# Optimization experiments

Hardware: AMD Instinct MI355X
Metric: run time of the kernel (lower is better)

Reference implementation:

```python
import jax, jax.numpy as jnp
import numpy as np

C, T, V, H, DQ = 64, 128, 25, 3, 32  # channels, frames, joints, heads, qkv_dim
EPS = 1e-5
LRELU_SLOPE = 0.1


def pos_embed(channels, num_frames, num_joints):
    # DSTA-Net style sinusoidal Pos_Embed: position index is the joint id, tiled over frames
    pos = np.tile(np.arange(num_joints, dtype=np.float32), num_frames)[:, None]  # (T*V, 1)
    div = np.exp(np.arange(0, channels, 2, dtype=np.float32) * -(np.log(10000.0) / channels))
    pe = np.zeros((num_frames * num_joints, channels), dtype=np.float32)
    pe[:, 0::2] = np.sin(pos * div)
    pe[:, 1::2] = np.cos(pos * div)
    pe = pe.reshape(num_frames, num_joints, channels).transpose(2, 0, 1)[None]  # (1, C, T, V)
    return jnp.asarray(pe)


def batchnorm2d(x, gamma, beta):
    # training-mode BN over (N, T, V) per channel, biased variance (torch default)
    m = x.mean(axis=(0, 2, 3), keepdims=True)
    v = x.var(axis=(0, 2, 3), keepdims=True)
    return (x - m) * jax.lax.rsqrt(v + EPS) * gamma[None, :, None, None] + beta[None, :, None, None]


def setup_inputs() -> dict:
    key = jax.random.key(0)
    ks = jax.random.split(key, 4)
    N = 64
    return {
        "x": jax.random.normal(ks[0], (N, C, T, V), jnp.float32),
        "Wqkv": jax.random.normal(ks[1], (2 * H * DQ, C), jnp.float32) * 0.05,   # 1x1 conv weight
        "bqkv": jnp.zeros((2 * H * DQ,), jnp.float32),
        "alphas": jnp.ones((1, H, 1, 1), jnp.float32),
        "att0s": jax.random.uniform(ks[2], (1, H, V, V), jnp.float32) / V,
        "Wout": jax.random.normal(ks[3], (C, H * C, 1, 5), jnp.float32) * 0.02,  # (1,5) temporal conv
        "bout": jnp.zeros((C,), jnp.float32),
        "gamma": jnp.ones((C,), jnp.float32),
        "beta": jnp.zeros((C,), jnp.float32),
    }


def reference(x, Wqkv, bqkv, alphas, att0s, Wout, bout, gamma, beta):
    N = x.shape[0]
    xs = x + pos_embed(C, T, V)                                   # pes(x) + x
    qk = jnp.einsum('nctv,oc->notv', xs, Wqkv) + bqkv[None, :, None, None]
    qk = qk.reshape(N, 2 * H, DQ, T, V)
    q, k = qk[:, :H], qk[:, H:]
    # tanh-gated joint-attention, no softmax
    att = jnp.tanh(jnp.einsum('nhctu,nhctv->nhuv', q, k) / (DQ * T)) * alphas + att0s
    y = jnp.einsum('nctu,nhuv->nhctv', x, att).reshape(N, H * C, T, V)
    y = jax.lax.conv_general_dilated(
        y, Wout, window_strides=(1, 1), padding=((0, 0), (2, 2)),
        dimension_numbers=('NCHW', 'OIHW', 'NCHW')) + bout[None, :, None, None]
    y = batchnorm2d(y, gamma, beta)
    return jax.nn.leaky_relu(y + x, LRELU_SLOPE)                  # ress is identity (in==out)
```

## Files before the change

kernel.cpp:

```cpp
#include <hip/hip_runtime.h>
#include <hip/hip_bf16.h>


#define WS_ATT    0
#define WS_STATS  120000
#define WS_WBF    120128
#define WS_WP     150848
#define WS_BP     156992
#define WS_PE     157184
#define WS_SPART  158784
#define WS_ATTBF  166976

typedef __attribute__((ext_vector_type(8))) short short8;
typedef __attribute__((ext_vector_type(4))) float floatx4;

__device__ __forceinline__ float us2f(unsigned short u) {
    union { unsigned int i; float f; } w; w.i = ((unsigned int)u) << 16; return w.f;
}
__device__ __forceinline__ unsigned short f2us(float f) {
    __hip_bfloat16_raw r = __float2bfloat16(f); return r.x;
}

__device__ __forceinline__ int swz(int col, int byteoff) {
    return col * 128 + ((((byteoff >> 4) ^ (col & 7)) << 4) | (byteoff & 15));
}

__device__ __forceinline__ void bar_lgkm() {
    asm volatile("s_waitcnt lgkmcnt(0)" ::: "memory");
    __builtin_amdgcn_s_barrier();
}

__global__ void k_wprep(const float* __restrict__ Wout, const float* __restrict__ Wqkv,
                        const float* __restrict__ bqkv, unsigned short* __restrict__ Abf,
                        unsigned short* __restrict__ Wp, float* __restrict__ bp,
                        float* __restrict__ pe)
{
    int i = blockIdx.x * 256 + threadIdx.x;
    if (i < 61440) {
        int tap = i / 12288, rem = i % 12288;
        int o = rem / 192, hc = rem % 192;
        Abf[i] = f2us(Wout[o * 960 + hc * 5 + tap]);
    } else if (i < 73728) {
        int j = i - 61440;
        int np = j >> 6, c = j & 63;
        int h = np >> 6, qk = (np >> 5) & 1, cp = np & 31;
        Wp[j] = f2us(Wqkv[(qk * 96 + h * 32 + cp) * 64 + c]);
    } else if (i < 73920) {
        int np = i - 73728;
        int h = np >> 6, qk = (np >> 5) & 1, cp = np & 31;
        bp[np] = bqkv[qk * 96 + h * 32 + cp];
    } else if (i < 75520) {
        int e = i - 73920;
        int c = e / 25, v = e % 25;
        int ii = c >> 1;
        float d = expf(-(float)(2 * ii) * (9.210340371976184f / 64.0f));
        float a = (float)v * d;
        pe[e] = (c & 1) ? cosf(a) : sinf(a);
    }
}

#define CPAD 112

__global__ __launch_bounds__(256, 2) void k_att(
    const float* __restrict__ x, const unsigned short* __restrict__ Wp,
    const float* __restrict__ bp, const float* __restrict__ peg,
    float* __restrict__ att_raw)
{
    __shared__ unsigned short xs_s[2][CPAD * 64];
    __shared__ unsigned short qk_s[3 * CPAD * 64];
    __shared__ float pe_s[1600];

    const int tid  = threadIdx.x;
    const int lane = tid & 63, wv = tid >> 6;
    const int l16  = lane & 15, quad = lane >> 4;
    const int n    = blockIdx.y;
    const int tb0  = blockIdx.x * 16;

    const int col_a = lane;
    const int col_b = 64 + lane;
    const int va = (col_a < 25) ? col_a : (col_a < 50 ? col_a - 25 : col_a - 50);
    const int vb = (col_b < 75) ? col_b - 50 : col_b - 75;
    char* qkb = (char*)qk_s;

    float ra0[8], ra1[8], rb0[8], rb1[8];

#define LOADCH(CH) do {                                                         \
    const int g0_ = (tb0 + (CH) * 4) * 25;                                      \
    _Pragma("unroll")                                                           \
    for (int cp8 = 0; cp8 < 8; ++cp8) {                                         \
        const float* xp0_ = x + (size_t)(n * 64 + (wv * 8 + cp8) * 2) * 3200 + g0_; \
        const float* xp1_ = xp0_ + 3200;                                        \
        ra0[cp8] = xp0_[col_a]; ra1[cp8] = xp1_[col_a];                         \
        if (lane < 36) { rb0[cp8] = xp0_[col_b]; rb1[cp8] = xp1_[col_b]; }      \
    } } while (0)

    LOADCH(0);

    for (int e = tid; e < 1600; e += 256) pe_s[e] = peg[e];

    short8 afrag[3][2];
    float  biasr[3][4];
    #pragma unroll
    for (int mt = 0; mt < 3; ++mt) {
        int row = (3 * wv + mt) * 16 + l16;
        #pragma unroll
        for (int kk = 0; kk < 2; ++kk)
            afrag[mt][kk] = *(const short8*)(Wp + row * 64 + kk * 32 + quad * 8);
        #pragma unroll
        for (int reg = 0; reg < 4; ++reg)
            biasr[mt][reg] = bp[(3 * wv + mt) * 16 + quad * 4 + reg];
    }

    floatx4 qacc[3][2][2];
    #pragma unroll
    for (int h = 0; h < 3; ++h)
        #pragma unroll
        for (int a = 0; a < 2; ++a)
            #pragma unroll
            for (int b = 0; b < 2; ++b)
                qacc[h][a][b] = (floatx4){0.0f, 0.0f, 0.0f, 0.0f};

    bar_lgkm();

    #pragma unroll
    for (int ch = 0; ch < 4; ++ch) {
        char* xsb = (char*)xs_s[ch & 1];

        #pragma unroll
        for (int cp8 = 0; cp8 < 8; ++cp8) {
            const int cpair = wv * 8 + cp8, c0 = cpair * 2;
            unsigned int pk =
                (unsigned int)f2us(ra0[cp8] + pe_s[c0 * 25 + va]) |
                ((unsigned int)f2us(ra1[cp8] + pe_s[c0 * 25 + 25 + va]) << 16);
            *(unsigned int*)(xsb + swz(col_a, cpair * 4)) = pk;
            if (lane < 36) {
                pk = (unsigned int)f2us(rb0[cp8] + pe_s[c0 * 25 + vb]) |
                     ((unsigned int)f2us(rb1[cp8] + pe_s[c0 * 25 + 25 + vb]) << 16);
                *(unsigned int*)(xsb + swz(col_b, cpair * 4)) = pk;
            }
        }
        if (ch < 3) LOADCH(ch + 1);
        bar_lgkm();

        #pragma unroll
        for (int nt = 0; nt < 7; ++nt) {
            const int col = nt * 16 + l16;
            short8 b0 = *(const short8*)(xsb + swz(col, quad * 16));
            short8 b1 = *(const short8*)(xsb + swz(col, 64 + quad * 16));
            #pragma unroll
            for (int mt = 0; mt < 3; ++mt) {
                floatx4 acc = (floatx4){0.0f, 0.0f, 0.0f, 0.0f};
                acc = __builtin_amdgcn_mfma_f32_16x16x32_bf16(afrag[mt][0], b0, acc, 0, 0, 0);
                acc = __builtin_amdgcn_mfma_f32_16x16x32_bf16(afrag[mt][1], b1, acc, 0, 0, 0);
                const int np  = (3 * wv + mt) * 16 + quad * 4;
                const int h   = np >> 6;
                const int off = (np & 63) * 2;
                unsigned long long pk =
                      (unsigned long long)f2us(acc[0] + biasr[mt][0])
                    | ((unsigned long long)f2us(acc[1] + biasr[mt][1]) << 16)
                    | ((unsigned long long)f2us(acc[2] + biasr[mt][2]) << 32)
                    | ((unsigned long long)f2us(acc[3] + biasr[mt][3]) << 48);
                *(unsigned long long*)(qkb + h * (CPAD * 128) + swz(col, off)) = pk;
            }
        }
        bar_lgkm();

        const int tcol = wv * 25;
        #pragma unroll
        for (int h = 0; h < 3; ++h) {
            char* qh = qkb + h * (CPAD * 128);
            short8 qa0 = *(const short8*)(qh + swz(tcol + l16,      quad * 16));
            short8 qa1 = *(const short8*)(qh + swz(tcol + 16 + l16, quad * 16));
            short8 kb0 = *(const short8*)(qh + swz(tcol + l16,      64 + quad * 16));
            short8 kb1 = *(const short8*)(qh + swz(tcol + 16 + l16, 64 + quad * 16));
            qacc[h][0][0] = __builtin_amdgcn_mfma_f32_16x16x32_bf16(qa0, kb0, qacc[h][0][0], 0, 0, 0);
            qacc[h][0][1] = __builtin_amdgcn_mfma_f32_16x16x32_bf16(qa0, kb1, qacc[h][0][1], 0, 0, 0);
            qacc[h][1][0] = __builtin_amdgcn_mfma_f32_16x16x32_bf16(qa1, kb0, qacc[h][1][0], 0, 0, 0);
            qacc[h][1][1] = __builtin_amdgcn_mfma_f32_16x16x32_bf16(qa1, kb1, qacc[h][1][1], 0, 0, 0);
        }
    }

    __syncthreads();
    float* att_s = (float*)qk_s;
    for (int e = tid; e < 1875; e += 256) att_s[e] = 0.0f;
    __syncthreads();
    #pragma unroll
    for (int h = 0; h < 3; ++h) {
        #pragma unroll
        for (int ut = 0; ut < 2; ++ut) {
            #pragma unroll
            for (int vt = 0; vt < 2; ++vt) {
                const int v = vt * 16 + l16;
                if (v < 25) {
                    const int ub = ut * 16 + quad * 4;
                    #pragma unroll
                    for (int reg = 0; reg < 4; ++reg) {
                        const int u = ub + reg;
                        if (u < 25)
                            atomicAdd(&att_s[h * 625 + u * 25 + v], qacc[h][ut][vt][reg]);
                    }
                }
            }
        }
    }
    __syncthreads();
    for (int e = tid; e < 1875; e += 256)
        atomicAdd(&att_raw[(size_t)n * 1875 + e], att_s[e]);
}

__global__ void k_attfin(const float* __restrict__ att_raw,
                         unsigned short* __restrict__ attbf,
                         const float* __restrict__ alphas,
                         const float* __restrict__ att0s)
{
    int idx = blockIdx.x * 256 + threadIdx.x;
    if (idx >= 64 * 3 * 25 * 40) return;
    int u = idx % 40;
    int r = idx / 40;
    int v = r % 25;
    int nh = r / 25;
    int h = nh % 3;
    unsigned short val = 0;
    if (u < 25) {
        float a = att_raw[nh * 625 + u * 25 + v];
        val = f2us(tanhf(a * (1.0f / 4096.0f)) * alphas[h] + att0s[h * 625 + u * 25 + v]);
    }
    attbf[idx] = val;
}

__global__ __launch_bounds__(256, 2) void k_conv(
    const float* __restrict__ x, const unsigned short* __restrict__ Abf,
    const float* __restrict__ bout, const unsigned short* __restrict__ attbf,
    float* __restrict__ out, float* __restrict__ spart)
{
    __shared__ unsigned short yT[11136];
    __shared__ unsigned short x_sb[4096];
    __shared__ unsigned short attT[3000];
    __shared__ float stats_s[128];

    const int tid = threadIdx.x;
    const int lane = tid & 63, wv = tid >> 6;
    const int quad = lane >> 4, l16 = lane & 15;
    const int n = blockIdx.y;
    const int t0 = blockIdx.x * 2;
    char* xsb = (char*)x_sb;

    const int o0 = wv * 16;
    short8 areg[5][6];
    const unsigned short* apb = Abf + (o0 + l16) * 192 + quad * 8;
    #pragma unroll
    for (int tap = 0; tap < 5; ++tap)
        #pragma unroll
        for (int kk = 0; kk < 6; ++kk)
            areg[tap][kk] = *(const short8*)(apb + tap * 12288 + kk * 32);
    float bo[4];
    #pragma unroll
    for (int reg = 0; reg < 4; ++reg) bo[reg] = bout[o0 + quad * 4 + reg];

    if (tid < 128) stats_s[tid] = 0.0f;

    for (int e = tid; e < 896; e += 256) {
        int c = e / 14, r = e % 14;
        int t = r / 7, u = 25 + r % 7;
        *(unsigned short*)(xsb + swz(c, (t * 32 + u) * 2)) = 0;
    }
    for (int e = tid; e < 1600; e += 256) {
        int c = e / 25, j = e % 25;
        const float2 xv = *(const float2*)(x + (size_t)(n * 64 + c) * 3200 + t0 * 25 + 2 * j);
        int i0 = 2 * j, i1 = i0 + 1;
        int p0 = (i0 / 25) * 32 + (i0 % 25);
        int p1 = (i1 / 25) * 32 + (i1 % 25);
        *(unsigned short*)(xsb + swz(c, p0 * 2)) = f2us(xv.x);
        *(unsigned short*)(xsb + swz(c, p1 * 2)) = f2us(xv.y);
    }
    {
        const uint4* src = (const uint4*)(attbf + (size_t)n * 3000);
        uint4* dst = (uint4*)attT;
        for (int e = tid; e < 375; e += 256) dst[e] = src[e];
    }
    for (int e = tid; e < 1536; e += 256) {
        int t = e / 768, r = e % 768;
        int vi = r / 192, hc = r % 192;
        int vv = (vi < 2) ? vi : (25 + vi);
        int phys = (t * 29 + vv) * 192 + (((hc >> 3) ^ (vv & 7)) << 3) + (hc & 7);
        yT[phys] = 0;
    }
    __syncthreads();

    {
        const int c0 = wv * 16;
        const int crow = c0 + l16;
        short8 af[2];
        #pragma unroll
        for (int t = 0; t < 2; ++t)
            af[t] = *(const short8*)(xsb + swz(crow, (t * 32 + quad * 8) * 2));
        short8 bfr[3][2];
        #pragma unroll
        for (int h = 0; h < 3; ++h)
            #pragma unroll
            for (int nt = 0; nt < 2; ++nt) {
                int v = nt * 16 + l16; if (v > 24) v = 24;
                bfr[h][nt] = *(const short8*)&attT[(h * 25 + v) * 40 + quad * 8];
            }
        #pragma unroll
        for (int t = 0; t < 2; ++t)
            #pragma unroll
            for (int h = 0; h < 3; ++h)
                #pragma unroll
                for (int nt = 0; nt < 2; ++nt) {
                    floatx4 d = (floatx4){0.0f, 0.0f, 0.0f, 0.0f};
                    d = __builtin_amdgcn_mfma_f32_16x16x32_bf16(af[t], bfr[h][nt], d, 0, 0, 0);
                    const int v = nt * 16 + l16;
                    if (v < 25) {
                        const int vv = v + 2;
                        const int hc = h * 64 + c0 + quad * 4;
                        const int phys = (t * 29 + vv) * 192 + (((hc >> 3) ^ (vv & 7)) << 3) + (hc & 7);
                        unsigned long long pk =
                              (unsigned long long)f2us(d[0])
                            | ((unsigned long long)f2us(d[1]) << 16)
                            | ((unsigned long long)f2us(d[2]) << 32)
                            | ((unsigned long long)f2us(d[3]) << 48);
                        *(unsigned long long*)&yT[phys] = pk;
                    }
                }
    }

    bar_lgkm();

    #pragma unroll
    for (int np = 0; np < 2; ++np) {
        const int colA = np * 32 + l16;
        const int colB = np * 32 + 16 + l16;
        const bool okA = colA < 50, okB = colB < 50;
        const int ccA = okA ? colA : 49, ccB = okB ? colB : 49;
        const int tcA = ccA / 25, vcA = ccA % 25;
        const int tcB = ccB / 25, vcB = ccB % 25;
        floatx4 accA = {0,0,0,0}, accB = {0,0,0,0};
        #pragma unroll
        for (int tap = 0; tap < 5; ++tap) {
            const int vvA = vcA + tap, vvB = vcB + tap;
            const int roA = (tcA * 29 + vvA) * 192, vxA = vvA & 7;
            const int roB = (tcB * 29 + vvB) * 192, vxB = vvB & 7;
            #pragma unroll
            for (int kk = 0; kk < 6; ++kk) {
                short8 bA = *(const short8*)&yT[roA + (((kk * 4 + quad) ^ vxA) << 3)];
                short8 bB = *(const short8*)&yT[roB + (((kk * 4 + quad) ^ vxB) << 3)];
                accA = __builtin_amdgcn_mfma_f32_16x16x32_bf16(areg[tap][kk], bA, accA, 0, 0, 0);
                accB = __builtin_amdgcn_mfma_f32_16x16x32_bf16(areg[tap][kk], bB, accB, 0, 0, 0);
            }
        }

#define EPIS(ACC, OK, TC, VC)                                                  \
        do {                                                                   \
            float vr[4];                                                       \
            _Pragma("unroll")                                                  \
            for (int reg = 0; reg < 4; ++reg)                                  \
                vr[reg] = (OK) ? ACC[reg] + bo[reg] : 0.0f;                    \
            if (OK) {                                                          \
                float* op = out + (size_t)(n * 64 + o0 + quad * 4) * 3200      \
                            + (t0 + (TC)) * 25 + (VC);                         \
                _Pragma("unroll")                                              \
                for (int reg = 0; reg < 4; ++reg)                              \
                    op[(size_t)reg * 3200] = vr[reg];                          \
            }                                                                  \
            _Pragma("unroll")                                                  \
            for (int reg = 0; reg < 4; ++reg) {                                \
                float s1 = vr[reg], s2 = vr[reg] * vr[reg];                    \
                _Pragma("unroll")                                              \
                for (int m = 1; m < 16; m <<= 1) {                             \
                    s1 += __shfl_xor(s1, m);                                   \
                    s2 += __shfl_xor(s2, m);                                   \
                }                                                              \
                if (l16 == 0) {                                                \
                    atomicAdd(&stats_s[o0 + quad * 4 + reg], s1);              \
                    atomicAdd(&stats_s[64 + o0 + quad * 4 + reg], s2);         \
                }                                                              \
            }                                                                  \
        } while (0)

        EPIS(accA, okA, tcA, vcA);
        EPIS(accB, okB, tcB, vcB);
#undef EPIS
    }

    __syncthreads();
    if (tid < 128)
        atomicAdd(&spart[(size_t)blockIdx.x * 128 + tid], stats_s[tid]);
}

__global__ void k_statsred(const float* __restrict__ spart, float* __restrict__ stats)
{
    int o = threadIdx.x;
    float s = 0.0f;
    #pragma unroll 8
    for (int t = 0; t < 64; ++t) s += spart[t * 128 + o];
    stats[o] = s;
}

__global__ void k_final(const float* __restrict__ stats, const float4* __restrict__ x4,
                        const float* __restrict__ gamma, const float* __restrict__ beta,
                        float4* __restrict__ out4)
{
    int idx = blockIdx.x * 256 + threadIdx.x;
    if (idx >= 3276800) return;
    int o = (idx / 800) & 63;
    const float inv = 1.0f / 204800.0f;
    float m   = stats[o] * inv;
    float ex2 = stats[64 + o] * inv;
    float var = ex2 - m * m;
    float r = rsqrtf(var + 1e-5f);
    float g = gamma[o], bb = beta[o];
    float4 v = out4[idx];
    float4 xx = x4[idx];
    float4 res;
    float t;
    t = (v.x - m) * r * g + bb + xx.x; res.x = fmaxf(t, 0.1f * t);
    t = (v.y - m) * r * g + bb + xx.y; res.y = fmaxf(t, 0.1f * t);
    t = (v.z - m) * r * g + bb + xx.z; res.z = fmaxf(t, 0.1f * t);
    t = (v.w - m) * r * g + bb + xx.w; res.w = fmaxf(t, 0.1f * t);
    out4[idx] = res;
}

extern "C" void kernel_launch(void* const* d_in, const int* in_sizes, int n_in,
                              void* d_out, int out_size, void* d_ws, size_t ws_size,
                              hipStream_t stream)
{
    const float* x      = (const float*)d_in[0];
    const float* Wqkv   = (const float*)d_in[1];
    const float* bqkv   = (const float*)d_in[2];
    const float* alphas = (const float*)d_in[3];
    const float* att0s  = (const float*)d_in[4];
    const float* Wout   = (const float*)d_in[5];
    const float* bout   = (const float*)d_in[6];
    const float* gamma  = (const float*)d_in[7];
    const float* beta   = (const float*)d_in[8];
    float* ws  = (float*)d_ws;
    float* out = (float*)d_out;
    unsigned short* Abf   = (unsigned short*)(ws + WS_WBF);
    unsigned short* Wp    = (unsigned short*)(ws + WS_WP);
    float*          bp    = ws + WS_BP;
    float*          pe    = ws + WS_PE;
    float*          spart = ws + WS_SPART;
    unsigned short* attbf = (unsigned short*)(ws + WS_ATTBF);

    hipMemsetAsync(d_ws, 0, (size_t)120000 * sizeof(float), stream);
    hipMemsetAsync(spart, 0, (size_t)8192 * sizeof(float), stream);

    k_wprep   <<<296, 256, 0, stream>>>(Wout, Wqkv, bqkv, Abf, Wp, bp, pe);
    k_att     <<<dim3(8, 64),  256, 0, stream>>>(x, Wp, bp, pe, ws + WS_ATT);
    k_attfin  <<<750, 256, 0, stream>>>(ws + WS_ATT, attbf, alphas, att0s);
    k_conv    <<<dim3(64, 64), 256, 0, stream>>>(x, Abf, bout, attbf, out, spart);
    k_statsred<<<1, 128, 0, stream>>>(spart, ws + WS_STATS);
    k_final   <<<12800, 256, 0, stream>>>(ws + WS_STATS, (const float4*)x,
                                          gamma, beta, (float4*)out);
}
```

Measured before the change: 307.8 us.

## Make conv blocks loop over 8 frame pairs with prefetched x and fused stats

k_conv now has each block handle 16 frames as 8 iterations over frame pairs, instead of launching one block per pair. Each block loads the conv weights into registers once and reuses them across iterations, and it prefetches the next pair's x into registers while the MFMA conv runs. BN statistics are kept in registers and reduced once at the end, then atomically added straight into the global stats, which removes the spart buffer, its memset and the k_statsred launch. The trade-off is fewer blocks (512 instead of 4096), which gives less parallelism and wave-level latency hiding, plus more register pressure from the rx prefetch buffers.

```diff
diff --git a/kernel.cpp b/kernel.cpp
--- a/kernel.cpp
+++ b/kernel.cpp
@@ -8,7 +8,6 @@
 #define WS_WP     150848
 #define WS_BP     156992
 #define WS_PE     157184
-#define WS_SPART  158784
 #define WS_ATTBF  166976
 
 typedef __attribute__((ext_vector_type(8))) short short8;
@@ -231,7 +230,7 @@
 __global__ __launch_bounds__(256, 2) void k_conv(
     const float* __restrict__ x, const unsigned short* __restrict__ Abf,
     const float* __restrict__ bout, const unsigned short* __restrict__ attbf,
-    float* __restrict__ out, float* __restrict__ spart)
+    float* __restrict__ out, float* __restrict__ stats_g)
 {
     __shared__ unsigned short yT[11136];
     __shared__ unsigned short x_sb[4096];
@@ -242,17 +241,22 @@
     const int lane = tid & 63, wv = tid >> 6;
     const int quad = lane >> 4, l16 = lane & 15;
     const int n = blockIdx.y;
-    const int t0 = blockIdx.x * 2;
+    const int tb0 = blockIdx.x * 16;
     char* xsb = (char*)x_sb;
 
     const int o0 = wv * 16;
     short8 areg[5][6];
-    const unsigned short* apb = Abf + (o0 + l16) * 192 + quad * 8;
-    #pragma unroll
-    for (int tap = 0; tap < 5; ++tap)
-        #pragma unroll
-        for (int kk = 0; kk < 6; ++kk)
-            areg[tap][kk] = *(const short8*)(apb + tap * 12288 + kk * 32);
+    {
+        const unsigned short* apb = Abf + (o0 + l16) * 192 + quad * 8;
+        #pragma unroll
+        for (int tap = 0; tap < 5; ++tap)
+            #pragma unroll
+            for (int kk = 0; kk < 6; ++kk) {
+                const unsigned short* ap = apb + tap * 12288 + kk * 32;
+                asm volatile("global_load_dwordx4 %0, %1, off"
+                             : "=&v"(areg[tap][kk]) : "v"(ap));
+            }
+    }
     float bo[4];
     #pragma unroll
     for (int reg = 0; reg < 4; ++reg) bo[reg] = bout[o0 + quad * 4 + reg];
@@ -263,15 +267,6 @@
         int c = e / 14, r = e % 14;
         int t = r / 7, u = 25 + r % 7;
         *(unsigned short*)(xsb + swz(c, (t * 32 + u) * 2)) = 0;
-    }
-    for (int e = tid; e < 1600; e += 256) {
-        int c = e / 25, j = e % 25;
-        const float2 xv = *(const float2*)(x + (size_t)(n * 64 + c) * 3200 + t0 * 25 + 2 * j);
-        int i0 = 2 * j, i1 = i0 + 1;
-        int p0 = (i0 / 25) * 32 + (i0 % 25);
-        int p1 = (i1 / 25) * 32 + (i1 % 25);
-        *(unsigned short*)(xsb + swz(c, p0 * 2)) = f2us(xv.x);
-        *(unsigned short*)(xsb + swz(c, p1 * 2)) = f2us(xv.y);
     }
     {
         const uint4* src = (const uint4*)(attbf + (size_t)n * 3000);
@@ -285,116 +280,153 @@
         int phys = (t * 29 + vv) * 192 + (((hc >> 3) ^ (vv & 7)) << 3) + (hc & 7);
         yT[phys] = 0;
     }
+
+    float2 rx[7];
+#define LOADX(P) do {                                                           \
+    const int t0_ = tb0 + (P) * 2;                                              \
+    _Pragma("unroll")                                                           \
+    for (int i = 0; i < 7; ++i) {                                               \
+        int e = tid + i * 256;                                                  \
+        if (e < 1600) {                                                         \
+            int c_ = e / 25, j_ = e % 25;                                       \
+            rx[i] = *(const float2*)(x + (size_t)(n * 64 + c_) * 3200           \
+                                     + t0_ * 25 + 2 * j_);                      \
+        }                                                                       \
+    } } while (0)
+
+    LOADX(0);
+
     __syncthreads();
-
-    {
-        const int c0 = wv * 16;
-        const int crow = c0 + l16;
-        short8 af[2];
-        #pragma unroll
-        for (int t = 0; t < 2; ++t)
-            af[t] = *(const short8*)(xsb + swz(crow, (t * 32 + quad * 8) * 2));
-        short8 bfr[3][2];
-        #pragma unroll
-        for (int h = 0; h < 3; ++h)
-            #pragma unroll
-            for (int nt = 0; nt < 2; ++nt) {
-                int v = nt * 16 + l16; if (v > 24) v = 24;
-                bfr[h][nt] = *(const short8*)&attT[(h * 25 + v) * 40 + quad * 8];
-            }
-        #pragma unroll
-        for (int t = 0; t < 2; ++t)
-            #pragma unroll
-            for (int h = 0; h < 3; ++h)
+    asm volatile("s_waitcnt vmcnt(0)" ::: "memory");
+    __builtin_amdgcn_sched_barrier(0);
+
+    short8 bfr[3][2];
+    #pragma unroll
+    for (int h = 0; h < 3; ++h)
+        #pragma unroll
+        for (int nt = 0; nt < 2; ++nt) {
+            int v = nt * 16 + l16; if (v > 24) v = 24;
+            bfr[h][nt] = *(const short8*)&attT[(h * 25 + v) * 40 + quad * 8];
+        }
+
+    float s1[4] = {0,0,0,0}, s2[4] = {0,0,0,0};
+
+    #pragma unroll 1
+    for (int p = 0; p < 8; ++p) {
+        const int t0 = tb0 + p * 2;
+
+        #pragma unroll
+        for (int i = 0; i < 7; ++i) {
+            int e = tid + i * 256;
+            if (e < 1600) {
+                int c_ = e / 25, j_ = e % 25;
+                int i0 = 2 * j_, i1 = i0 + 1;
+                int p0 = (i0 / 25) * 32 + (i0 % 25);
+                int p1 = (i1 / 25) * 32 + (i1 % 25);
+                *(unsigned short*)(xsb + swz(c_, p0 * 2)) = f2us(rx[i].x);
+                *(unsigned short*)(xsb + swz(c_, p1 * 2)) = f2us(rx[i].y);
+            }
+        }
+        bar_lgkm();
+
+        {
+            const int c0 = wv * 16;
+            const int crow = c0 + l16;
+            short8 af[2];
+            #pragma unroll
+            for (int t = 0; t < 2; ++t)
+                af[t] = *(const short8*)(xsb + swz(crow, (t * 32 + quad * 8) * 2));
+            #pragma unroll
+            for (int t = 0; t < 2; ++t)
                 #pragma unroll
-                for (int nt = 0; nt < 2; ++nt) {
-                    floatx4 d = (floatx4){0.0f, 0.0f, 0.0f, 0.0f};
-                    d = __builtin_amdgcn_mfma_f32_16x16x32_bf16(af[t], bfr[h][nt], d, 0, 0, 0);
-                    const int v = nt * 16 + l16;
-                    if (v < 25) {
-                        const int vv = v + 2;
-                        const int hc = h * 64 + c0 + quad * 4;
-                        const int phys = (t * 29 + vv) * 192 + (((hc >> 3) ^ (vv & 7)) << 3) + (hc & 7);
-                        unsigned long long pk =
-                              (unsigned long long)f2us(d[0])
-                            | ((unsigned long long)f2us(d[1]) << 16)
-                            | ((unsigned long long)f2us(d[2]) << 32)
-                            | ((unsigned long long)f2us(d[3]) << 48);
-                        *(unsigned long long*)&yT[phys] = pk;
+                for (int h = 0; h < 3; ++h)
+                    #pragma unroll
+                    for (int nt = 0; nt < 2; ++nt) {
+                        floatx4 d = (floatx4){0.0f, 0.0f, 0.0f, 0.0f};
+                        d = __builtin_amdgcn_mfma_f32_16x16x32_bf16(af[t], bfr[h][nt], d, 0, 0, 0);
+                        const int v = nt * 16 + l16;
+                        if (v < 25) {
+                            const int vv = v + 2;
+                            const int hc = h * 64 + c0 + quad * 4;
+                            const int phys = (t * 29 + vv) * 192 + (((hc >> 3) ^ (vv & 7)) << 3) + (hc & 7);
+                            unsigned long long pk =
+                                  (unsigned long long)f2us(d[0])
+                                | ((unsigned long long)f2us(d[1]) << 16)
+                                | ((unsigned long long)f2us(d[2]) << 32)
+                                | ((unsigned long long)f2us(d[3]) << 48);
+                            *(unsigned long long*)&yT[phys] = pk;
+                        }
                     }
+        }
+        bar_lgkm();
+
+        if (p < 7) LOADX(p + 1);
+
+        #pragma unroll
+        for (int np = 0; np < 2; ++np) {
+            const int colA = np * 32 + l16;
+            const int colB = np * 32 + 16 + l16;
+            const bool okA = colA < 50, okB = colB < 50;
+            const int ccA = okA ? colA : 49, ccB = okB ? colB : 49;
+            const int tcA = ccA / 25, vcA = ccA % 25;
+            const int tcB = ccB / 25, vcB = ccB % 25;
+            floatx4 accA = {0,0,0,0}, accB = {0,0,0,0};
+            #pragma unroll
+            for (int tap = 0; tap < 5; ++tap) {
+                const int vvA = vcA + tap, vvB = vcB + tap;
+                const int roA = (tcA * 29 + vvA) * 192, vxA = vvA & 7;
+                const int roB = (tcB * 29 + vvB) * 192, vxB = vvB & 7;
+                #pragma unroll
+                for (int kk = 0; kk < 6; ++kk) {
+                    short8 bA = *(const short8*)&yT[roA + (((kk * 4 + quad) ^ vxA) << 3)];
+                    short8 bB = *(const short8*)&yT[roB + (((kk * 4 + quad) ^ vxB) << 3)];
+                    accA = __builtin_amdgcn_mfma_f32_16x16x32_bf16(areg[tap][kk], bA, accA, 0, 0, 0);
+                    accB = __builtin_amdgcn_mfma_f32_16x16x32_bf16(areg[tap][kk], bB, accB, 0, 0, 0);
                 }
-    }
-
-    bar_lgkm();
-
-    #pragma unroll
-    for (int np = 0; np < 2; ++np) {
-        const int colA = np * 32 + l16;
-        const int colB = np * 32 + 16 + l16;
-        const bool okA = colA < 50, okB = colB < 50;
-        const int ccA = okA ? colA : 49, ccB = okB ? colB : 49;
-        const int tcA = ccA / 25, vcA = ccA % 25;
-        const int tcB = ccB / 25, vcB = ccB % 25;
-        floatx4 accA = {0,0,0,0}, accB = {0,0,0,0};
-        #pragma unroll
-        for (int tap = 0; tap < 5; ++tap) {
-            const int vvA = vcA + tap, vvB = vcB + tap;
-            const int roA = (tcA * 29 + vvA) * 192, vxA = vvA & 7;
-            const int roB = (tcB * 29 + vvB) * 192, vxB = vvB & 7;
-            #pragma unroll
-            for (int kk = 0; kk < 6; ++kk) {
-                short8 bA = *(const short8*)&yT[roA + (((kk * 4 + quad) ^ vxA) << 3)];
-                short8 bB = *(const short8*)&yT[roB + (((kk * 4 + quad) ^ vxB) << 3)];
-                accA = __builtin_amdgcn_mfma_f32_16x16x32_bf16(areg[tap][kk], bA, accA, 0, 0, 0);
-                accB = __builtin_amdgcn_mfma_f32_16x16x32_bf16(areg[tap][kk], bB, accB, 0, 0, 0);
-            }
-        }
+            }
 
 #define EPIS(ACC, OK, TC, VC)                                                  \
-        do {                                                                   \
-            float vr[4];                                                       \
-            _Pragma("unroll")                                                  \
-            for (int reg = 0; reg < 4; ++reg)                                  \
-                vr[reg] = (OK) ? ACC[reg] + bo[reg] : 0.0f;                    \
-            if (OK) {                                                          \
-                float* op = out + (size_t)(n * 64 + o0 + quad * 4) * 3200      \
-                            + (t0 + (TC)) * 25 + (VC);                         \
+            do {                                                               \
+                float vr[4];                                                   \
                 _Pragma("unroll")                                              \
                 for (int reg = 0; reg < 4; ++reg)                              \
-                    op[(size_t)reg * 3200] = vr[reg];                          \
-            }                                                                  \
-            _Pragma("unroll")                                                  \
-            for (int reg = 0; reg < 4; ++reg) {                                \
-                float s1 = vr[reg], s2 = vr[reg] * vr[reg];                    \
+                    vr[reg] = (OK) ? ACC[reg] + bo[reg] : 0.0f;                \
+                if (OK) {                                                      \
+                    float* op = out + (size_t)(n * 64 + o0 + quad * 4) * 3200  \
+                                + (t0 + (TC)) * 25 + (VC);                     \
+                    _Pragma("unroll")                                          \
+                    for (int reg = 0; reg < 4; ++reg)                          \
+                        op[(size_t)reg * 3200] = vr[reg];                      \
+                }                                                              \
                 _Pragma("unroll")                                              \
-                for (int m = 1; m < 16; m <<= 1) {                             \
-                    s1 += __shfl_xor(s1, m);                                   \
-                    s2 += __shfl_xor(s2, m);                                   \
+                for (int reg = 0; reg < 4; ++reg) {                            \
+                    s1[reg] += vr[reg];                                        \
+                    s2[reg] = fmaf(vr[reg], vr[reg], s2[reg]);                 \
                 }                                                              \
-                if (l16 == 0) {                                                \
-                    atomicAdd(&stats_s[o0 + quad * 4 + reg], s1);              \
-                    atomicAdd(&stats_s[64 + o0 + quad * 4 + reg], s2);         \
-                }                                                              \
-            }                                                                  \
-        } while (0)
-
-        EPIS(accA, okA, tcA, vcA);
-        EPIS(accB, okB, tcB, vcB);
+            } while (0)
+
+            EPIS(accA, okA, tcA, vcA);
+            EPIS(accB, okB, tcB, vcB);
 #undef EPIS
-    }
-
+        }
+    }
+
+    #pragma unroll
+    for (int reg = 0; reg < 4; ++reg) {
+        float a = s1[reg], b = s2[reg];
+        #pragma unroll
+        for (int m = 1; m < 16; m <<= 1) {
+            a += __shfl_xor(a, m);
+            b += __shfl_xor(b, m);
+        }
+        if (l16 == 0) {
+            atomicAdd(&stats_s[o0 + quad * 4 + reg], a);
+            atomicAdd(&stats_s[64 + o0 + quad * 4 + reg], b);
+        }
+    }
     __syncthreads();
     if (tid < 128)
-        atomicAdd(&spart[(size_t)blockIdx.x * 128 + tid], stats_s[tid]);
-}
-
-__global__ void k_statsred(const float* __restrict__ spart, float* __restrict__ stats)
-{
-    int o = threadIdx.x;
-    float s = 0.0f;
-    #pragma unroll 8
-    for (int t = 0; t < 64; ++t) s += spart[t * 128 + o];
-    stats[o] = s;
+        atomicAdd(&stats_g[tid], stats_s[tid]);
 }
 
 __global__ void k_final(const float* __restrict__ stats, const float4* __restrict__ x4,
@@ -440,17 +472,14 @@
     unsigned short* Wp    = (unsigned short*)(ws + WS_WP);
     float*          bp    = ws + WS_BP;
     float*          pe    = ws + WS_PE;
-    float*          spart = ws + WS_SPART;
     unsigned short* attbf = (unsigned short*)(ws + WS_ATTBF);
 
-    hipMemsetAsync(d_ws, 0, (size_t)120000 * sizeof(float), stream);
-    hipMemsetAsync(spart, 0, (size_t)8192 * sizeof(float), stream);
+    hipMemsetAsync(d_ws, 0, (size_t)(120000 + 128) * sizeof(float), stream);
 
     k_wprep   <<<296, 256, 0, stream>>>(Wout, Wqkv, bqkv, Abf, Wp, bp, pe);
     k_att     <<<dim3(8, 64),  256, 0, stream>>>(x, Wp, bp, pe, ws + WS_ATT);
     k_attfin  <<<750, 256, 0, stream>>>(ws + WS_ATT, attbf, alphas, att0s);
-    k_conv    <<<dim3(64, 64), 256, 0, stream>>>(x, Abf, bout, attbf, out, spart);
-    k_statsred<<<1, 128, 0, stream>>>(spart, ws + WS_STATS);
+    k_conv    <<<dim3(8, 64),  256, 0, stream>>>(x, Abf, bout, attbf, out, ws + WS_STATS);
     k_final   <<<12800, 256, 0, stream>>>(ws + WS_STATS, (const float4*)x,
                                           gamma, beta, (float4*)out);
 }
```

Measured after the change: 441.6 us. +43.4%, slower.

## Raise k_conv occupancy: defer weight loads, single accumulator, batched stats reduction

Applied to the files above, without the earlier changes.

Moves the per-wave weight register load (areg) to after the attention-mix phase so its live range no longer overlaps the staging code, and raises launch bounds from 2 to 3 blocks per SM. The conv loop now uses one accumulator per column tile instead of two interleaved ones, which lowers register pressure. BN statistic partials are accumulated in registers across all column tiles and reduced with shuffles and atomics once instead of per tile. The aim is higher occupancy and fewer shuffle/atomic operations, at the cost of less MFMA interleaving (a single dependent accumulator chain) and possible spills under the tighter register budget.

```diff
diff --git a/kernel.cpp b/kernel.cpp
--- a/kernel.cpp
+++ b/kernel.cpp
@@ -228,7 +228,7 @@
     attbf[idx] = val;
 }
 
-__global__ __launch_bounds__(256, 2) void k_conv(
+__global__ __launch_bounds__(256, 3) void k_conv(
     const float* __restrict__ x, const unsigned short* __restrict__ Abf,
     const float* __restrict__ bout, const unsigned short* __restrict__ attbf,
     float* __restrict__ out, float* __restrict__ spart)
@@ -239,23 +239,9 @@
     __shared__ float stats_s[128];
 
     const int tid = threadIdx.x;
-    const int lane = tid & 63, wv = tid >> 6;
-    const int quad = lane >> 4, l16 = lane & 15;
     const int n = blockIdx.y;
     const int t0 = blockIdx.x * 2;
     char* xsb = (char*)x_sb;
-
-    const int o0 = wv * 16;
-    short8 areg[5][6];
-    const unsigned short* apb = Abf + (o0 + l16) * 192 + quad * 8;
-    #pragma unroll
-    for (int tap = 0; tap < 5; ++tap)
-        #pragma unroll
-        for (int kk = 0; kk < 6; ++kk)
-            areg[tap][kk] = *(const short8*)(apb + tap * 12288 + kk * 32);
-    float bo[4];
-    #pragma unroll
-    for (int reg = 0; reg < 4; ++reg) bo[reg] = bout[o0 + quad * 4 + reg];
 
     if (tid < 128) stats_s[tid] = 0.0f;
 
@@ -286,6 +272,9 @@
         yT[phys] = 0;
     }
     __syncthreads();
+
+    const int lane = tid & 63, wv = tid >> 6;
+    const int quad = lane >> 4, l16 = lane & 15;
 
     {
         const int c0 = wv * 16;
@@ -325,64 +314,68 @@
                 }
     }
 
+    const int o0 = wv * 16;
+    short8 areg[5][6];
+    const unsigned short* apb = Abf + (o0 + l16) * 192 + quad * 8;
+    #pragma unroll
+    for (int tap = 0; tap < 5; ++tap)
+        #pragma unroll
+        for (int kk = 0; kk < 6; ++kk)
+            areg[tap][kk] = *(const short8*)(apb + tap * 12288 + kk * 32);
+    float bo[4];
+    #pragma unroll
+    for (int reg = 0; reg < 4; ++reg) bo[reg] = bout[o0 + quad * 4 + reg];
+
     bar_lgkm();
 
-    #pragma unroll
-    for (int np = 0; np < 2; ++np) {
-        const int colA = np * 32 + l16;
-        const int colB = np * 32 + 16 + l16;
-        const bool okA = colA < 50, okB = colB < 50;
-        const int ccA = okA ? colA : 49, ccB = okB ? colB : 49;
-        const int tcA = ccA / 25, vcA = ccA % 25;
-        const int tcB = ccB / 25, vcB = ccB % 25;
-        floatx4 accA = {0,0,0,0}, accB = {0,0,0,0};
+    float s1[4] = {0, 0, 0, 0}, s2[4] = {0, 0, 0, 0};
+    #pragma unroll
+    for (int nt = 0; nt < 4; ++nt) {
+        int col = nt * 16 + l16;
+        const bool ok = col < 50;
+        if (col > 49) col = 49;
+        const int tc = col / 25, vc = col % 25;
+        floatx4 acc = (floatx4){0.0f, 0.0f, 0.0f, 0.0f};
         #pragma unroll
         for (int tap = 0; tap < 5; ++tap) {
-            const int vvA = vcA + tap, vvB = vcB + tap;
-            const int roA = (tcA * 29 + vvA) * 192, vxA = vvA & 7;
-            const int roB = (tcB * 29 + vvB) * 192, vxB = vvB & 7;
+            const int vv = vc + tap;
+            const int ro = (tc * 29 + vv) * 192, vx = vv & 7;
             #pragma unroll
             for (int kk = 0; kk < 6; ++kk) {
-                short8 bA = *(const short8*)&yT[roA + (((kk * 4 + quad) ^ vxA) << 3)];
-                short8 bB = *(const short8*)&yT[roB + (((kk * 4 + quad) ^ vxB) << 3)];
-                accA = __builtin_amdgcn_mfma_f32_16x16x32_bf16(areg[tap][kk], bA, accA, 0, 0, 0);
-                accB = __builtin_amdgcn_mfma_f32_16x16x32_bf16(areg[tap][kk], bB, accB, 0, 0, 0);
+                short8 b = *(const short8*)&yT[ro + (((kk * 4 + quad) ^ vx) << 3)];
+                acc = __builtin_amdgcn_mfma_f32_16x16x32_bf16(areg[tap][kk], b, acc, 0, 0, 0);
             }
         }
-
-#define EPIS(ACC, OK, TC, VC)                                                  \
-        do {                                                                   \
-            float vr[4];                                                       \
-            _Pragma("unroll")                                                  \
-            for (int reg = 0; reg < 4; ++reg)                                  \
-                vr[reg] = (OK) ? ACC[reg] + bo[reg] : 0.0f;                    \
-            if (OK) {                                                          \
-                float* op = out + (size_t)(n * 64 + o0 + quad * 4) * 3200      \
-                            + (t0 + (TC)) * 25 + (VC);                         \
-                _Pragma("unroll")                                              \
-                for (int reg = 0; reg < 4; ++reg)                              \
-                    op[(size_t)reg * 3200] = vr[reg];                          \
-            }                                                                  \
-            _Pragma("unroll")                                                  \
-            for (int reg = 0; reg < 4; ++reg) {                                \
-                float s1 = vr[reg], s2 = vr[reg] * vr[reg];                    \
-                _Pragma("unroll")                                              \
-                for (int m = 1; m < 16; m <<= 1) {                             \
-                    s1 += __shfl_xor(s1, m);                                   \
-                    s2 += __shfl_xor(s2, m);                                   \
-                }                                                              \
-                if (l16 == 0) {                                                \
-                    atomicAdd(&stats_s[o0 + quad * 4 + reg], s1);              \
-                    atomicAdd(&stats_s[64 + o0 + quad * 4 + reg], s2);         \
-                }                                                              \
-            }                                                                  \
-        } while (0)
-
-        EPIS(accA, okA, tcA, vcA);
-        EPIS(accB, okB, tcB, vcB);
-#undef EPIS
-    }
-
+        float vr[4];
+        #pragma unroll
+        for (int reg = 0; reg < 4; ++reg)
+            vr[reg] = ok ? acc[reg] + bo[reg] : 0.0f;
+        if (ok) {
+            float* op = out + (size_t)(n * 64 + o0 + quad * 4) * 3200 + (t0 + tc) * 25 + vc;
+            #pragma unroll
+            for (int reg = 0; reg < 4; ++reg)
+                op[(size_t)reg * 3200] = vr[reg];
+        }
+        #pragma unroll
+        for (int reg = 0; reg < 4; ++reg) {
+            s1[reg] += vr[reg];
+            s2[reg] = fmaf(vr[reg], vr[reg], s2[reg]);
+        }
+    }
+
+    #pragma unroll
+    for (int reg = 0; reg < 4; ++reg) {
+        float a = s1[reg], b = s2[reg];
+        #pragma unroll
+        for (int m = 1; m < 16; m <<= 1) {
+            a += __shfl_xor(a, m);
+            b += __shfl_xor(b, m);
+        }
+        if (l16 == 0) {
+            atomicAdd(&stats_s[o0 + quad * 4 + reg], a);
+            atomicAdd(&stats_s[64 + o0 + quad * 4 + reg], b);
+        }
+    }
     __syncthreads();
     if (tid < 128)
         atomicAdd(&spart[(size_t)blockIdx.x * 128 + tid], stats_s[tid]);
```

After: 268.5 us. -12.8%, faster.
